# Kernel optimization log

Measured on AMD Instinct MI355X. Metric: run time of the kernel, lower is better.

## Reference

```python
import jax, jax.numpy as jnp
import numpy as np
import math

B, L, D, H = 2, 2048, 512, 8
DH = D // H  # 64
MAX_SEQ = 2048


def setup_inputs() -> dict:
    key = jax.random.key(0)
    ks = jax.random.split(key, 9)
    rn = lambda k, sh: jax.random.normal(k, sh, dtype=jnp.float32)
    w_scale = 0.02
    # causal mask: 1 where attention is disallowed (upper triangle)
    causal = jnp.triu(jnp.ones((L, L), jnp.float32), k=1)[None, None]
    return {
        "q_in": rn(ks[0], (B, L, D)),
        "k_in": rn(ks[1], (B, L, D)),
        "v_in": rn(ks[2], (B, L, D)),
        "mask": causal,
        "Wq": rn(ks[3], (D, D)) * w_scale,
        "bq": jnp.zeros((D,), jnp.float32),
        "Wk": rn(ks[4], (D, D)) * w_scale,
        "bk": jnp.zeros((D,), jnp.float32),
        "Wv": rn(ks[5], (D, D)) * w_scale,
        "bv": jnp.zeros((D,), jnp.float32),
        "Wfc": rn(ks[6], (D, D)) * w_scale,
        "bfc": jnp.zeros((D,), jnp.float32),
        "E": rn(ks[7], (MAX_SEQ, DH)),  # relative position embedding (non-trainable buffer)
    }


def _heads(x, W, b):
    # [B,L,D] -> [B,H,L,DH]
    y = x @ W + b
    return y.reshape(x.shape[0], x.shape[1], H, DH).transpose(0, 2, 1, 3)


def _qe_mask(len_q):
    # keep[l, m] = (m >= len_q - 1 - l); zeros out invalid relative offsets
    rows = jnp.arange(len_q)[:, None]
    cols = jnp.arange(len_q)[None, :]
    return (cols >= (len_q - 1 - rows)).astype(jnp.float32)


def _skew(QE):
    # Music-Transformer skewing: [B,H,L,M] -> pad left on last dim ->
    # reshape swapping last two dims -> drop first row => Srel [B,H,M,L]
    b, h, l, m = QE.shape
    padded = jnp.pad(QE, ((0, 0), (0, 0), (0, 0), (1, 0)))  # [b,h,l,m+1]
    reshaped = padded.reshape(b, h, m + 1, l)
    return reshaped[:, :, 1:, :]  # [b,h,m,l]


def reference(q_in, k_in, v_in, mask, Wq, bq, Wk, bk, Wv, bv, Wfc, bfc, E):
    q = _heads(q_in, Wq, bq)  # [B,H,L,DH]
    k = _heads(k_in, Wk, bk)
    v = _heads(v_in, Wv, bv)
    len_q = q.shape[2]
    # left embedding slice: E[max(0, MAX_SEQ - len_q):]
    e = E[max(0, MAX_SEQ - len_q):, :]  # [M, DH], M == len_q here
    QE = jnp.einsum('bhld,md->bhlm', q, e)
    QE = QE * _qe_mask(len_q)  # broadcast [L,M] over [B,H,L,M]
    Srel = _skew(QE)  # [B,H,L,L]
    QKt = jnp.einsum('bhld,bhmd->bhlm', q, k)
    logits = (QKt + Srel) / np.sqrt(DH).astype(np.float32)
    logits = logits + mask * (-1e9)
    attn_weights = jax.nn.softmax(logits, axis=-1)
    attn = jnp.einsum('bhlm,bhmd->bhld', attn_weights, v)
    out = attn.transpose(0, 2, 1, 3).reshape(q_in.shape[0], -1, D)
    out = out @ Wfc + bfc
    return out, attn_weights
```

## Files before the change

kernel.cpp:

```cpp
#include <hip/hip_runtime.h>
#include <math.h>

#define L 2048
#define DMODEL 512
#define NH 8
#define DH 64
#define NROWS 4096

typedef __attribute__((ext_vector_type(4))) float f32x4;
typedef __attribute__((ext_vector_type(8))) short s16x8;

#define MFMA(a, b, c) __builtin_amdgcn_mfma_f32_16x16x32_bf16(a, b, c, 0, 0, 0)

static __device__ __forceinline__ ushort f2b(float f) {
    union { float f; unsigned u; } v; v.f = f;
    unsigned r = v.u + 0x7FFF + ((v.u >> 16) & 1);
    return (ushort)(r >> 16);
}

__global__ __launch_bounds__(256)
void cvt_bf16(const float* __restrict__ in, ushort* __restrict__ out, int n8) {
    int i = blockIdx.x * 256 + threadIdx.x;
    if (i < n8) {
        float4 a = *reinterpret_cast<const float4*>(&in[(size_t)i * 8]);
        float4 b = *reinterpret_cast<const float4*>(&in[(size_t)i * 8 + 4]);
        ushort4 o0; o0.x = f2b(a.x); o0.y = f2b(a.y); o0.z = f2b(a.z); o0.w = f2b(a.w);
        ushort4 o1; o1.x = f2b(b.x); o1.y = f2b(b.y); o1.z = f2b(b.z); o1.w = f2b(b.w);
        *reinterpret_cast<ushort4*>(&out[(size_t)i * 8]) = o0;
        *reinterpret_cast<ushort4*>(&out[(size_t)i * 8 + 4]) = o1;
    }
}

__global__ __launch_bounds__(256)
void transpose_w(const float* __restrict__ W0, const float* __restrict__ W1,
                 const float* __restrict__ W2, const float* __restrict__ W3,
                 ushort* __restrict__ T0, ushort* __restrict__ T1,
                 ushort* __restrict__ T2, ushort* __restrict__ T3) {
    const int z = blockIdx.z;
    const float* W = z == 0 ? W0 : (z == 1 ? W1 : (z == 2 ? W2 : W3));
    ushort* T = z == 0 ? T0 : (z == 1 ? T1 : (z == 2 ? T2 : T3));
    __shared__ float Ls[64][65];
    const int tid = threadIdx.x;
    const int k0 = blockIdx.y * 64, n0 = blockIdx.x * 64;
    #pragma unroll
    for (int i = 0; i < 4; ++i) {
        int kk = (tid >> 4) + i * 16, n4 = (tid & 15) * 4;
        float4 v = *reinterpret_cast<const float4*>(&W[(size_t)(k0 + kk) * 512 + n0 + n4]);
        Ls[kk][n4] = v.x; Ls[kk][n4 + 1] = v.y; Ls[kk][n4 + 2] = v.z; Ls[kk][n4 + 3] = v.w;
    }
    __syncthreads();
    #pragma unroll
    for (int i = 0; i < 4; ++i) {
        int nn = (tid >> 4) + i * 16, k4 = (tid & 15) * 4;
        ushort4 o;
        o.x = f2b(Ls[k4 + 0][nn]); o.y = f2b(Ls[k4 + 1][nn]);
        o.z = f2b(Ls[k4 + 2][nn]); o.w = f2b(Ls[k4 + 3][nn]);
        *reinterpret_cast<ushort4*>(&T[(size_t)(n0 + nn) * 512 + k0 + k4]) = o;
    }
}

__global__ __launch_bounds__(256)
void gemm_bf16(const void* __restrict__ A0, const void* __restrict__ A1,
               const ushort* __restrict__ W0, const ushort* __restrict__ W1,
               const float* __restrict__ b0, const float* __restrict__ b1,
               void* o0, void* o1, int a_f32, int mode) {
    const int z = blockIdx.z;
    const void* A   = z == 0 ? A0 : A1;
    const ushort* Wt = z == 0 ? W0 : W1;
    const float* bias = z == 0 ? b0 : b1;
    void* outp = z == 0 ? o0 : o1;

    __shared__ ushort As[128][40];
    __shared__ ushort Bs[64][40];
    const int tid = threadIdx.x;
    const int w = tid >> 6, lane = tid & 63, g = lane >> 4, c = lane & 15;
    const int m0 = blockIdx.y * 128, n0 = blockIdx.x * 64;

    f32x4 acc[2][4];
    #pragma unroll
    for (int rs = 0; rs < 2; ++rs)
        #pragma unroll
        for (int cs = 0; cs < 4; ++cs) acc[rs][cs] = (f32x4){0.f, 0.f, 0.f, 0.f};

    float bsv[4];
    #pragma unroll
    for (int cs = 0; cs < 4; ++cs) bsv[cs] = bias[n0 + 16 * cs + c];

    for (int k0 = 0; k0 < 512; k0 += 32) {
        {
            int row = tid >> 1, kh = (tid & 1) * 16;
            if (a_f32) {
                const float* p = (const float*)A + (size_t)(m0 + row) * 512 + k0 + kh;
                ushort tmp[16];
                #pragma unroll
                for (int q4 = 0; q4 < 4; ++q4) {
                    float4 f = *reinterpret_cast<const float4*>(p + q4 * 4);
                    tmp[q4 * 4 + 0] = f2b(f.x); tmp[q4 * 4 + 1] = f2b(f.y);
                    tmp[q4 * 4 + 2] = f2b(f.z); tmp[q4 * 4 + 3] = f2b(f.w);
                }
                *reinterpret_cast<uint4*>(&As[row][kh]) = *reinterpret_cast<uint4*>(&tmp[0]);
                *reinterpret_cast<uint4*>(&As[row][kh + 8]) = *reinterpret_cast<uint4*>(&tmp[8]);
            } else {
                const ushort* p = (const ushort*)A + (size_t)(m0 + row) * 512 + k0 + kh;
                uint4 x0 = *reinterpret_cast<const uint4*>(p);
                uint4 x1 = *reinterpret_cast<const uint4*>(p + 8);
                *reinterpret_cast<uint4*>(&As[row][kh]) = x0;
                *reinterpret_cast<uint4*>(&As[row][kh + 8]) = x1;
            }
        }
        {
            int n = tid >> 2, kh = (tid & 3) * 8;
            uint4 x = *reinterpret_cast<const uint4*>(&Wt[(size_t)(n0 + n) * 512 + k0 + kh]);
            *reinterpret_cast<uint4*>(&Bs[n][kh]) = x;
        }
        __syncthreads();
        s16x8 af[2], bf[4];
        #pragma unroll
        for (int rs = 0; rs < 2; ++rs)
            af[rs] = *reinterpret_cast<const s16x8*>(&As[32 * w + 16 * rs + c][8 * g]);
        #pragma unroll
        for (int cs = 0; cs < 4; ++cs)
            bf[cs] = *reinterpret_cast<const s16x8*>(&Bs[16 * cs + c][8 * g]);
        #pragma unroll
        for (int rs = 0; rs < 2; ++rs)
            #pragma unroll
            for (int cs = 0; cs < 4; ++cs)
                acc[rs][cs] = MFMA(af[rs], bf[cs], acc[rs][cs]);
        __syncthreads();
    }
    #pragma unroll
    for (int rs = 0; rs < 2; ++rs)
        #pragma unroll
        for (int cs = 0; cs < 4; ++cs)
            #pragma unroll
            for (int r = 0; r < 4; ++r) {
                int row = m0 + 32 * w + 16 * rs + 4 * g + r;
                int n = n0 + 16 * cs + c;
                float v = acc[rs][cs][r] + bsv[cs];
                int bb = row >> 11, l = row & 2047, hh = n >> 6, dh = n & 63;
                if (mode == 0) {
                    ((float*)outp)[(size_t)row * 512 + n] = v;
                } else if (mode == 1) {
                    ((ushort*)outp)[(((size_t)bb * NH + hh) * L + l) * DH + dh] = f2b(v);
                } else {
                    ((ushort*)outp)[(((size_t)bb * NH + hh) * DH + dh) * L + l] = f2b(v);
                }
            }
}

__global__ __launch_bounds__(256, 3)
void attn(const ushort* __restrict__ qws, const ushort* __restrict__ kws,
          const ushort* __restrict__ vtg, const ushort* __restrict__ Ebf,
          float* __restrict__ attnw, ushort* __restrict__ ows,
          float* __restrict__ linvg) {
    __shared__ float Ored[4][32][68];
    __shared__ float lred[4][32];
    __shared__ float linvs[32];

    const int tid = threadIdx.x;
    const int w = tid >> 6, lane = tid & 63, g = lane >> 4, c = lane & 15;
    const int bid = blockIdx.x;
    const int bh = bid & 15;
    const int ib = 63 - (bid >> 4);
    const int b = bh >> 3, h = bh & 7;
    const int i0 = ib * 32;
    const int nt = ib + 1;

    const ushort* qb = qws + (size_t)bh * L * DH;
    const ushort* kb = kws + (size_t)bh * L * DH;
    const ushort* vt = vtg + (size_t)bh * DH * L;
    float* ab = attnw + (size_t)bh * L * L;

    ushort (*Pw)[40] = reinterpret_cast<ushort(*)[40]>(&Ored[w][0][0]);

    s16x8 aq[2][2];
    #pragma unroll
    for (int rs = 0; rs < 2; ++rs)
        #pragma unroll
        for (int ks = 0; ks < 2; ++ks)
            aq[rs][ks] = *reinterpret_cast<const s16x8*>(
                qb + (size_t)(i0 + 16 * rs + c) * DH + 32 * ks + 8 * g);

    f32x4 O[2][4];
    #pragma unroll
    for (int rs = 0; rs < 2; ++rs)
        #pragma unroll
        for (int cs = 0; cs < 4; ++cs) O[rs][cs] = (f32x4){0.f, 0.f, 0.f, 0.f};
    float lsum[2][4] = {};

    for (int t = w; t < nt; t += 4) {
        const int j0 = t * 32;
        const int rbase = L - 32 - i0 + j0;

        f32x4 TT[4][2];
        #pragma unroll
        for (int ct = 0; ct < 4; ++ct) {
            s16x8 be[2];
            int rg = rbase + 16 * ct + c;
            rg = rg > L - 1 ? L - 1 : rg;
            #pragma unroll
            for (int ks = 0; ks < 2; ++ks)
                be[ks] = *reinterpret_cast<const s16x8*>(
                    Ebf + (size_t)rg * DH + 32 * ks + 8 * g);
            #pragma unroll
            for (int rs = 0; rs < 2; ++rs) {
                f32x4 x = {0.f, 0.f, 0.f, 0.f};
                x = MFMA(aq[rs][0], be[0], x);
                x = MFMA(aq[rs][1], be[1], x);
                TT[ct][rs] = x;
            }
        }
        float rel[2][2][4];
        #pragma unroll
        for (int r = 0; r < 4; ++r) {
            const int u = c - 4 * g - r;
            const int src = (lane & 48) | ((15 + u) & 15);
            const bool hi = (u >= 1);
            #pragma unroll
            for (int rs = 0; rs < 2; ++rs)
                #pragma unroll
                for (int jh = 0; jh < 2; ++jh) {
                    const int b0 = jh - rs + 1;
                    float va = __shfl(TT[b0][rs][r], src);
                    float vb = __shfl(TT[b0 + 1][rs][r], src);
                    rel[rs][jh][r] = hi ? vb : va;
                }
        }
        f32x4 SK[2][2];
        {
            s16x8 bk[2][2];
            #pragma unroll
            for (int jh = 0; jh < 2; ++jh)
                #pragma unroll
                for (int ks = 0; ks < 2; ++ks)
                    bk[jh][ks] = *reinterpret_cast<const s16x8*>(
                        kb + (size_t)(j0 + 16 * jh + c) * DH + 32 * ks + 8 * g);
            #pragma unroll
            for (int rs = 0; rs < 2; ++rs)
                #pragma unroll
                for (int jh = 0; jh < 2; ++jh) {
                    f32x4 x = {0.f, 0.f, 0.f, 0.f};
                    x = MFMA(aq[rs][0], bk[jh][0], x);
                    x = MFMA(aq[rs][1], bk[jh][1], x);
                    SK[rs][jh] = x;
                }
        }
        #pragma unroll
        for (int rs = 0; rs < 2; ++rs)
            #pragma unroll
            for (int jh = 0; jh < 2; ++jh)
                #pragma unroll
                for (int r = 0; r < 4; ++r) {
                    const int il = 16 * rs + 4 * g + r;
                    const int jl = 16 * jh + c;
                    float s = (SK[rs][jh][r] + rel[rs][jh][r]) * 0.125f;
                    float p = (j0 + jl <= i0 + il) ? __expf(s) : 0.0f;
                    lsum[rs][r] += p;
                    ab[(size_t)(i0 + il) * L + j0 + jl] = p;
                    Pw[il][jl] = f2b(p);
                }
        s16x8 pa[2];
        #pragma unroll
        for (int rs2 = 0; rs2 < 2; ++rs2)
            pa[rs2] = *reinterpret_cast<const s16x8*>(&Pw[16 * rs2 + c][8 * g]);
        #pragma unroll
        for (int cs = 0; cs < 4; ++cs) {
            s16x8 vtb = *reinterpret_cast<const s16x8*>(
                vt + (size_t)(16 * cs + c) * L + j0 + 8 * g);
            #pragma unroll
            for (int rs2 = 0; rs2 < 2; ++rs2)
                O[rs2][cs] = MFMA(pa[rs2], vtb, O[rs2][cs]);
        }
    }

    #pragma unroll
    for (int rs = 0; rs < 2; ++rs)
        #pragma unroll
        for (int r = 0; r < 4; ++r) {
            float s = lsum[rs][r];
            s += __shfl_xor(s, 1); s += __shfl_xor(s, 2);
            s += __shfl_xor(s, 4); s += __shfl_xor(s, 8);
            if (c == 0) lred[w][16 * rs + 4 * g + r] = s;
        }
    #pragma unroll
    for (int rs2 = 0; rs2 < 2; ++rs2)
        #pragma unroll
        for (int cs = 0; cs < 4; ++cs)
            #pragma unroll
            for (int r = 0; r < 4; ++r)
                Ored[w][16 * rs2 + 4 * g + r][16 * cs + c] = O[rs2][cs][r];
    __syncthreads();
    if (tid < 32) {
        float l = lred[0][tid] + lred[1][tid] + lred[2][tid] + lred[3][tid];
        float inv = 1.0f / l;
        linvs[tid] = inv;
        linvg[(size_t)bh * L + i0 + tid] = inv;
    }
    __syncthreads();
    {
        const int i = tid >> 3, d8 = (tid & 7) * 8;
        const float inv = linvs[i];
        ushort o[8];
        #pragma unroll
        for (int e = 0; e < 8; ++e) {
            float a = Ored[0][i][d8 + e] + Ored[1][i][d8 + e]
                    + Ored[2][i][d8 + e] + Ored[3][i][d8 + e];
            o[e] = f2b(a * inv);
        }
        *reinterpret_cast<uint4*>(
            &ows[((size_t)b * L + i0 + i) * DMODEL + h * DH + d8]) =
            *reinterpret_cast<const uint4*>(&o[0]);
    }
}

__global__ __launch_bounds__(256)
void rescale(float* __restrict__ attnw, const float* __restrict__ linvg) {
    const int blk = blockIdx.x;
    const int bh = blk >> 11, i = blk & 2047;
    const float inv = linvg[(size_t)bh * L + i];
    float* rowp = attnw + ((size_t)bh * L + i) * L;
    const int c8 = threadIdx.x * 8;
    float4 a, b2;
    if (c8 <= i) {
        a  = *reinterpret_cast<const float4*>(rowp + c8);
        b2 = *reinterpret_cast<const float4*>(rowp + c8 + 4);
        a.x  = (c8 + 0 <= i) ? a.x  * inv : 0.f;
        a.y  = (c8 + 1 <= i) ? a.y  * inv : 0.f;
        a.z  = (c8 + 2 <= i) ? a.z  * inv : 0.f;
        a.w  = (c8 + 3 <= i) ? a.w  * inv : 0.f;
        b2.x = (c8 + 4 <= i) ? b2.x * inv : 0.f;
        b2.y = (c8 + 5 <= i) ? b2.y * inv : 0.f;
        b2.z = (c8 + 6 <= i) ? b2.z * inv : 0.f;
        b2.w = (c8 + 7 <= i) ? b2.w * inv : 0.f;
    } else {
        a = make_float4(0.f, 0.f, 0.f, 0.f);
        b2 = a;
    }
    *reinterpret_cast<float4*>(rowp + c8) = a;
    *reinterpret_cast<float4*>(rowp + c8 + 4) = b2;
}

extern "C" void kernel_launch(void* const* d_in, const int* in_sizes, int n_in,
                              void* d_out, int out_size, void* d_ws, size_t ws_size,
                              hipStream_t stream) {
    const float* q_in = (const float*)d_in[0];
    const float* k_in = (const float*)d_in[1];
    const float* v_in = (const float*)d_in[2];
    const float* Wq  = (const float*)d_in[4];
    const float* bq  = (const float*)d_in[5];
    const float* Wk  = (const float*)d_in[6];
    const float* bk  = (const float*)d_in[7];
    const float* Wv  = (const float*)d_in[8];
    const float* bv  = (const float*)d_in[9];
    const float* Wfc = (const float*)d_in[10];
    const float* bfc = (const float*)d_in[11];
    const float* E   = (const float*)d_in[12];

    float* out0  = (float*)d_out;
    float* attnw = out0 + (size_t)2 * L * DMODEL;

    const size_t NA = (size_t)NROWS * DMODEL;
    ushort* ws = (ushort*)d_ws;
    ushort* Ebf  = ws;
    ushort* Wqt  = Ebf + (size_t)L * DH;
    ushort* Wkt  = Wqt + 262144;
    ushort* Wvt  = Wkt + 262144;
    ushort* Wfct = Wvt + 262144;
    ushort* qws  = Wfct + 262144;
    ushort* kws  = qws + NA;
    ushort* vtg  = kws + NA;
    ushort* ows  = vtg + NA;
    float*  linvg = (float*)(ows + NA);

    cvt_bf16<<<dim3(64), 256, 0, stream>>>(E, Ebf, (int)(L * DH / 8));
    transpose_w<<<dim3(8, 8, 4), 256, 0, stream>>>(Wq, Wk, Wv, Wfc, Wqt, Wkt, Wvt, Wfct);
    gemm_bf16<<<dim3(8, 32, 2), 256, 0, stream>>>(q_in, k_in, Wqt, Wkt,
                                                  bq, bk, qws, kws, 1, 1);
    gemm_bf16<<<dim3(8, 32, 1), 256, 0, stream>>>(v_in, v_in, Wvt, Wvt,
                                                  bv, bv, vtg, vtg, 1, 2);
    attn<<<dim3(1024), 256, 0, stream>>>(qws, kws, vtg, Ebf, attnw, ows, linvg);
    rescale<<<dim3(32768), 256, 0, stream>>>(attnw, linvg);
    gemm_bf16<<<dim3(8, 32, 1), 256, 0, stream>>>(ows, ows, Wfct, Wfct,
                                                  bfc, bfc, out0, out0, 0, 0);
}
```

Before: 216.1 us.

## Stage attention probabilities through LDS for coalesced stores, merge QKV GEMM launches

The attention kernel now writes unnormalized probabilities into a per-wave LDS tile and then emits coalesced float4 row stores to the attention-weight matrix, replacing scattered scalar global stores. The block-to-row-tile mapping interleaves long and short causal tiles to balance load across CUs, and occupancy is raised to 4 blocks per SM with the S·K MFMA fused into the softmax loop to shrink live registers. The Q/K/V projections are merged into one 3-way launch using packed per-z modes, and rescale gains a fast path for fully unmasked 8-element chunks. This adds an extra LDS round trip and sync, and the higher occupancy target risks register spills.

Result: slower. 260.8 us (+20.6%).

```diff
diff --git a/kernel.cpp b/kernel.cpp
--- a/kernel.cpp
+++ b/kernel.cpp
@@ -61,14 +61,18 @@
 
 __global__ __launch_bounds__(256)
 void gemm_bf16(const void* __restrict__ A0, const void* __restrict__ A1,
+               const void* __restrict__ A2,
                const ushort* __restrict__ W0, const ushort* __restrict__ W1,
+               const ushort* __restrict__ W2,
                const float* __restrict__ b0, const float* __restrict__ b1,
-               void* o0, void* o1, int a_f32, int mode) {
+               const float* __restrict__ b2,
+               void* o0, void* o1, void* o2, int a_f32, int modes) {
     const int z = blockIdx.z;
-    const void* A   = z == 0 ? A0 : A1;
-    const ushort* Wt = z == 0 ? W0 : W1;
-    const float* bias = z == 0 ? b0 : b1;
-    void* outp = z == 0 ? o0 : o1;
+    const void* A   = z == 0 ? A0 : (z == 1 ? A1 : A2);
+    const ushort* Wt = z == 0 ? W0 : (z == 1 ? W1 : W2);
+    const float* bias = z == 0 ? b0 : (z == 1 ? b1 : b2);
+    void* outp = z == 0 ? o0 : (z == 1 ? o1 : o2);
+    const int mode = (modes >> (4 * z)) & 15;
 
     __shared__ ushort As[128][40];
     __shared__ ushort Bs[64][40];
@@ -148,7 +152,7 @@
             }
 }
 
-__global__ __launch_bounds__(256, 3)
+__global__ __launch_bounds__(256, 4)
 void attn(const ushort* __restrict__ qws, const ushort* __restrict__ kws,
           const ushort* __restrict__ vtg, const ushort* __restrict__ Ebf,
           float* __restrict__ attnw, ushort* __restrict__ ows,
@@ -161,7 +165,10 @@
     const int w = tid >> 6, lane = tid & 63, g = lane >> 4, c = lane & 15;
     const int bid = blockIdx.x;
     const int bh = bid & 15;
-    const int ib = 63 - (bid >> 4);
+    const int u = bid >> 4;
+    const int qd = u >> 4, v = u & 15;
+    const int ib = (qd == 0) ? 2 * v : (qd == 1) ? (63 - 2 * v)
+                 : (qd == 2) ? (2 * v + 1) : (62 - 2 * v);
     const int b = bh >> 3, h = bh & 7;
     const int i0 = ib * 32;
     const int nt = ib + 1;
@@ -171,7 +178,8 @@
     const ushort* vt = vtg + (size_t)bh * DH * L;
     float* ab = attnw + (size_t)bh * L * L;
 
-    ushort (*Pw)[40] = reinterpret_cast<ushort(*)[40]>(&Ored[w][0][0]);
+    float*  Ps = &Ored[w][0][0];
+    ushort* Pw = (ushort*)(Ps + 32 * 36);
 
     s16x8 aq[2][2];
     #pragma unroll
@@ -181,41 +189,37 @@
             aq[rs][ks] = *reinterpret_cast<const s16x8*>(
                 qb + (size_t)(i0 + 16 * rs + c) * DH + 32 * ks + 8 * g);
 
+    float lsum[2][4] = {};
     f32x4 O[2][4];
     #pragma unroll
     for (int rs = 0; rs < 2; ++rs)
         #pragma unroll
         for (int cs = 0; cs < 4; ++cs) O[rs][cs] = (f32x4){0.f, 0.f, 0.f, 0.f};
-    float lsum[2][4] = {};
 
     for (int t = w; t < nt; t += 4) {
         const int j0 = t * 32;
         const int rbase = L - 32 - i0 + j0;
-
         f32x4 TT[4][2];
         #pragma unroll
         for (int ct = 0; ct < 4; ++ct) {
-            s16x8 be[2];
             int rg = rbase + 16 * ct + c;
             rg = rg > L - 1 ? L - 1 : rg;
-            #pragma unroll
-            for (int ks = 0; ks < 2; ++ks)
-                be[ks] = *reinterpret_cast<const s16x8*>(
-                    Ebf + (size_t)rg * DH + 32 * ks + 8 * g);
+            s16x8 be0 = *reinterpret_cast<const s16x8*>(Ebf + (size_t)rg * DH + 8 * g);
+            s16x8 be1 = *reinterpret_cast<const s16x8*>(Ebf + (size_t)rg * DH + 32 + 8 * g);
             #pragma unroll
             for (int rs = 0; rs < 2; ++rs) {
                 f32x4 x = {0.f, 0.f, 0.f, 0.f};
-                x = MFMA(aq[rs][0], be[0], x);
-                x = MFMA(aq[rs][1], be[1], x);
+                x = MFMA(aq[rs][0], be0, x);
+                x = MFMA(aq[rs][1], be1, x);
                 TT[ct][rs] = x;
             }
         }
         float rel[2][2][4];
         #pragma unroll
         for (int r = 0; r < 4; ++r) {
-            const int u = c - 4 * g - r;
-            const int src = (lane & 48) | ((15 + u) & 15);
-            const bool hi = (u >= 1);
+            const int u2 = c - 4 * g - r;
+            const int src = (lane & 48) | ((15 + u2) & 15);
+            const bool hi = (u2 >= 1);
             #pragma unroll
             for (int rs = 0; rs < 2; ++rs)
                 #pragma unroll
@@ -226,43 +230,44 @@
                     rel[rs][jh][r] = hi ? vb : va;
                 }
         }
-        f32x4 SK[2][2];
-        {
-            s16x8 bk[2][2];
-            #pragma unroll
-            for (int jh = 0; jh < 2; ++jh)
-                #pragma unroll
-                for (int ks = 0; ks < 2; ++ks)
-                    bk[jh][ks] = *reinterpret_cast<const s16x8*>(
-                        kb + (size_t)(j0 + 16 * jh + c) * DH + 32 * ks + 8 * g);
-            #pragma unroll
-            for (int rs = 0; rs < 2; ++rs)
-                #pragma unroll
-                for (int jh = 0; jh < 2; ++jh) {
-                    f32x4 x = {0.f, 0.f, 0.f, 0.f};
-                    x = MFMA(aq[rs][0], bk[jh][0], x);
-                    x = MFMA(aq[rs][1], bk[jh][1], x);
-                    SK[rs][jh] = x;
-                }
-        }
+        s16x8 bk[2][2];
+        #pragma unroll
+        for (int jh = 0; jh < 2; ++jh)
+            #pragma unroll
+            for (int ks = 0; ks < 2; ++ks)
+                bk[jh][ks] = *reinterpret_cast<const s16x8*>(
+                    kb + (size_t)(j0 + 16 * jh + c) * DH + 32 * ks + 8 * g);
         #pragma unroll
         for (int rs = 0; rs < 2; ++rs)
             #pragma unroll
-            for (int jh = 0; jh < 2; ++jh)
+            for (int jh = 0; jh < 2; ++jh) {
+                f32x4 x = {0.f, 0.f, 0.f, 0.f};
+                x = MFMA(aq[rs][0], bk[jh][0], x);
+                x = MFMA(aq[rs][1], bk[jh][1], x);
                 #pragma unroll
                 for (int r = 0; r < 4; ++r) {
                     const int il = 16 * rs + 4 * g + r;
                     const int jl = 16 * jh + c;
-                    float s = (SK[rs][jh][r] + rel[rs][jh][r]) * 0.125f;
+                    float s = (x[r] + rel[rs][jh][r]) * 0.125f;
                     float p = (j0 + jl <= i0 + il) ? __expf(s) : 0.0f;
                     lsum[rs][r] += p;
-                    ab[(size_t)(i0 + il) * L + j0 + jl] = p;
-                    Pw[il][jl] = f2b(p);
+                    Ps[il * 36 + jl] = p;
+                    Pw[il * 40 + jl] = f2b(p);
                 }
+            }
+        {
+            const int row = lane >> 1, cb = (lane & 1) * 16;
+            float* dst = &ab[(size_t)(i0 + row) * L + j0 + cb];
+            const float* srcp = &Ps[row * 36 + cb];
+            #pragma unroll
+            for (int e = 0; e < 4; ++e)
+                *reinterpret_cast<float4*>(dst + 4 * e) =
+                    *reinterpret_cast<const float4*>(srcp + 4 * e);
+        }
         s16x8 pa[2];
         #pragma unroll
         for (int rs2 = 0; rs2 < 2; ++rs2)
-            pa[rs2] = *reinterpret_cast<const s16x8*>(&Pw[16 * rs2 + c][8 * g]);
+            pa[rs2] = *reinterpret_cast<const s16x8*>(&Pw[(16 * rs2 + c) * 40 + 8 * g]);
         #pragma unroll
         for (int cs = 0; cs < 4; ++cs) {
             s16x8 vtb = *reinterpret_cast<const s16x8*>(
@@ -282,13 +287,6 @@
             s += __shfl_xor(s, 4); s += __shfl_xor(s, 8);
             if (c == 0) lred[w][16 * rs + 4 * g + r] = s;
         }
-    #pragma unroll
-    for (int rs2 = 0; rs2 < 2; ++rs2)
-        #pragma unroll
-        for (int cs = 0; cs < 4; ++cs)
-            #pragma unroll
-            for (int r = 0; r < 4; ++r)
-                Ored[w][16 * rs2 + 4 * g + r][16 * cs + c] = O[rs2][cs][r];
     __syncthreads();
     if (tid < 32) {
         float l = lred[0][tid] + lred[1][tid] + lred[2][tid] + lred[3][tid];
@@ -297,6 +295,15 @@
         linvg[(size_t)bh * L + i0 + tid] = inv;
     }
     __syncthreads();
+
+    #pragma unroll
+    for (int rs2 = 0; rs2 < 2; ++rs2)
+        #pragma unroll
+        for (int cs = 0; cs < 4; ++cs)
+            #pragma unroll
+            for (int r = 0; r < 4; ++r)
+                Ored[w][16 * rs2 + 4 * g + r][16 * cs + c] = O[rs2][cs][r];
+    __syncthreads();
     {
         const int i = tid >> 3, d8 = (tid & 7) * 8;
         const float inv = linvs[i];
@@ -317,11 +324,16 @@
 void rescale(float* __restrict__ attnw, const float* __restrict__ linvg) {
     const int blk = blockIdx.x;
     const int bh = blk >> 11, i = blk & 2047;
-    const float inv = linvg[(size_t)bh * L + i];
-    float* rowp = attnw + ((size_t)bh * L + i) * L;
+    const float inv = linvg[((size_t)bh << 11) + i];
+    float* rowp = attnw + (((size_t)bh << 11) + i) * 2048;
     const int c8 = threadIdx.x * 8;
     float4 a, b2;
-    if (c8 <= i) {
+    if (c8 + 7 <= i) {
+        a  = *reinterpret_cast<const float4*>(rowp + c8);
+        b2 = *reinterpret_cast<const float4*>(rowp + c8 + 4);
+        a.x *= inv; a.y *= inv; a.z *= inv; a.w *= inv;
+        b2.x *= inv; b2.y *= inv; b2.z *= inv; b2.w *= inv;
+    } else if (c8 <= i) {
         a  = *reinterpret_cast<const float4*>(rowp + c8);
         b2 = *reinterpret_cast<const float4*>(rowp + c8 + 4);
         a.x  = (c8 + 0 <= i) ? a.x  * inv : 0.f;
@@ -374,12 +386,12 @@
 
     cvt_bf16<<<dim3(64), 256, 0, stream>>>(E, Ebf, (int)(L * DH / 8));
     transpose_w<<<dim3(8, 8, 4), 256, 0, stream>>>(Wq, Wk, Wv, Wfc, Wqt, Wkt, Wvt, Wfct);
-    gemm_bf16<<<dim3(8, 32, 2), 256, 0, stream>>>(q_in, k_in, Wqt, Wkt,
-                                                  bq, bk, qws, kws, 1, 1);
-    gemm_bf16<<<dim3(8, 32, 1), 256, 0, stream>>>(v_in, v_in, Wvt, Wvt,
-                                                  bv, bv, vtg, vtg, 1, 2);
+    gemm_bf16<<<dim3(8, 32, 3), 256, 0, stream>>>(q_in, k_in, v_in, Wqt, Wkt, Wvt,
+                                                  bq, bk, bv, qws, kws, vtg,
+                                                  1, 0x211);
     attn<<<dim3(1024), 256, 0, stream>>>(qws, kws, vtg, Ebf, attnw, ows, linvg);
     rescale<<<dim3(32768), 256, 0, stream>>>(attnw, linvg);
-    gemm_bf16<<<dim3(8, 32, 1), 256, 0, stream>>>(ows, ows, Wfct, Wfct,
-                                                  bfc, bfc, out0, out0, 0, 0);
-}
+    gemm_bf16<<<dim3(8, 32, 1), 256, 0, stream>>>(ows, ows, ows, Wfct, Wfct, Wfct,
+                                                  bfc, bfc, bfc, out0, out0, out0,
+                                                  0, 0x0);
+}
```
